# Performance work log

Hardware: AMD Instinct MI355X
Metric: run time of the kernel (lower is better)

Reference implementation:

```python
import jax, jax.numpy as jnp
import numpy as np
import itertools

GRID_SIZES = [0.01, 0.02, 0.04, 0.08, 0.16, 0.32, 0.64, 1.28]
OFFSETS = np.array(list(itertools.product([-1, 0, 1], repeat=3)), dtype=np.int32)  # [27,3]; index 13 = (0,0,0)
B, N, IN_DIM, HID, OUT_DIM = 2, 65536, 3, 32, 128


def make_neighbors(p, g):
    """Submanifold-conv neighbor tables for one grid scale.
    Returns nbr [27, b*n] int32 (flat point id or -1) and mask [27, b*n] bool.
    """
    b, n, _ = p.shape
    D = int(np.ceil(1.0 / g)) + 1  # static upper bound on spatial shape (p in [0,1))
    gc = jnp.floor(p / g).astype(jnp.int32)
    gc = gc - jnp.min(gc, axis=1, keepdims=True)  # per-batch min, as in torch code
    ids = jnp.arange(b * n, dtype=jnp.int32).reshape(b, n)
    bidx = jnp.arange(b, dtype=jnp.int32)[:, None]
    # deterministic voxel hash: one representative point id per occupied voxel
    grid = jnp.full((b, D, D, D), -1, jnp.int32)
    grid = grid.at[bidx, gc[..., 0], gc[..., 1], gc[..., 2]].max(ids)
    off = jnp.asarray(OFFSETS)
    nc = gc[None] + off[:, None, None, :]  # [27,b,n,3]
    valid = jnp.all((nc >= 0) & (nc < D), axis=-1)
    ncc = jnp.clip(nc, 0, D - 1)
    nbr = grid[bidx[None], ncc[..., 0], ncc[..., 1], ncc[..., 2]]  # [27,b,n]
    mask = valid & (nbr >= 0)
    nbr = nbr.at[13].set(ids)  # center tap is always the point itself
    mask = mask.at[13].set(True)
    return nbr.reshape(27, b * n), mask.reshape(27, b * n)


def subm_conv(f, W, bias, nbr, mask):
    """Submanifold 3x3x3 sparse conv on active sites.
    f [M,h]; W [27,h,h]; nbr/mask [27,M]. out[p] = bias + sum_k (f @ W_k)[nbr_k(p)] (masked).
    Scan over the 27 kernel taps keeps peak memory at O(M*h).
    """
    def step(acc, kin):
        Wk, nbrk, mk = kin
        acc = acc + jnp.where(mk[:, None], (f @ Wk)[nbrk], 0.0)
        return acc, None
    acc0 = jnp.zeros_like(f) + bias
    out, _ = jax.lax.scan(step, acc0, (W, nbr, mask))
    return out


def mssc_forward(p, w1, b1, w_mlp, b_mlp, w_conv, b_conv, w2, b2, neighbors):
    b, n, _ = p.shape
    pts = p @ w1 + b1  # mlp_1: [b,n,HID]
    outs = []
    for i in range(len(GRID_SIZES)):
        nbr, mask = neighbors[i]
        h0 = (pts @ w_mlp[i] + b_mlp[i]).reshape(b * n, HID)  # per-scale MLP
        h1 = subm_conv(h0, w_conv[2 * i], b_conv[2 * i], nbr, mask) + h0
        h2 = subm_conv(h1, w_conv[2 * i + 1], b_conv[2 * i + 1], nbr, mask) + h1
        outs.append(h2 + h0)  # features + features_batch residual
    feat = jnp.concatenate(outs, axis=1).reshape(b, n, HID * len(GRID_SIZES))
    return feat @ w2 + b2  # mlp_2


def setup_inputs():
    key = jax.random.key(0)
    ks = jax.random.split(key, 10)
    L = len(GRID_SIZES)
    return {
        "p": jax.random.uniform(ks[0], (B, N, IN_DIM), jnp.float32),
        "w1": jax.random.normal(ks[1], (IN_DIM, HID), jnp.float32) / np.sqrt(IN_DIM),
        "b1": 0.01 * jax.random.normal(ks[2], (HID,), jnp.float32),
        "w_mlp": jax.random.normal(ks[3], (L, HID, HID), jnp.float32) / np.sqrt(HID),
        "b_mlp": 0.01 * jax.random.normal(ks[4], (L, HID), jnp.float32),
        "w_conv": jax.random.normal(ks[5], (2 * L, 27, HID, HID), jnp.float32) / np.sqrt(27 * HID),
        "b_conv": 0.01 * jax.random.normal(ks[6], (2 * L, HID), jnp.float32),
        "w2": jax.random.normal(ks[7], (HID * L, OUT_DIM), jnp.float32) / np.sqrt(HID * L),
        "b2": 0.01 * jax.random.normal(ks[8], (OUT_DIM,), jnp.float32),
    }


def reference(p, w1, b1, w_mlp, b_mlp, w_conv, b_conv, w2, b2):
    neighbors = [make_neighbors(p, g) for g in GRID_SIZES]
    return mssc_forward(p, w1, b1, w_mlp, b_mlp, w_conv, b_conv, w2, b2, neighbors)
```

## Files before the change

### kernel.cpp

```cpp
#include <hip/hip_runtime.h>

#define MTOT 131072
#define NB   65536

typedef __attribute__((ext_vector_type(8))) __bf16 bf16x8;
typedef __attribute__((ext_vector_type(4))) __bf16 bf16x4;
typedef __attribute__((ext_vector_type(4))) float  f32x4;

__global__ void pmin_init_kernel(float* pmin){
    if (threadIdx.x < 6) pmin[threadIdx.x] = 2.0f;
}

__global__ void pmin_kernel(const float* __restrict__ p, float* __restrict__ pmin){
    int bi = blockIdx.y;
    float m0 = 2.f, m1 = 2.f, m2 = 2.f;
    for (int ni = blockIdx.x * blockDim.x + threadIdx.x; ni < NB; ni += gridDim.x * blockDim.x){
        const float* pp = p + ((size_t)bi * NB + ni) * 3;
        m0 = fminf(m0, pp[0]); m1 = fminf(m1, pp[1]); m2 = fminf(m2, pp[2]);
    }
    #pragma unroll
    for (int o = 32; o > 0; o >>= 1){
        m0 = fminf(m0, __shfl_down(m0, o, 64));
        m1 = fminf(m1, __shfl_down(m1, o, 64));
        m2 = fminf(m2, __shfl_down(m2, o, 64));
    }
    if ((threadIdx.x & 63) == 0){
        atomicMin((int*)(pmin + bi*3 + 0), __float_as_int(m0));
        atomicMin((int*)(pmin + bi*3 + 1), __float_as_int(m1));
        atomicMin((int*)(pmin + bi*3 + 2), __float_as_int(m2));
    }
}

template<int USE_LDS>
__global__ void scatter_kernel(const float* __restrict__ p, const float* __restrict__ pmin,
                               int* __restrict__ vgrid, int* __restrict__ gcbuf,
                               double gd, int D){
    extern __shared__ int lgrid[];
    int m  = blockIdx.x * blockDim.x + threadIdx.x;
    int bi = m >> 16;
    double px = (double)p[m*3], py = (double)p[m*3+1], pz = (double)p[m*3+2];
    int gx = (int)floor(px / gd) - (int)floor((double)pmin[bi*3+0] / gd);
    int gy = (int)floor(py / gd) - (int)floor((double)pmin[bi*3+1] / gd);
    int gz = (int)floor(pz / gd) - (int)floor((double)pmin[bi*3+2] / gd);
    gcbuf[m] = (gx << 20) | (gy << 10) | gz;
    int cell = (gx * D + gy) * D + gz;

    if (!USE_LDS){
        atomicMax(vgrid + bi * D * D * D + cell, m);
        return;
    }
    int ncell = D * D * D;
    for (int c = threadIdx.x; c < ncell; c += 256) lgrid[c] = -1;
    __syncthreads();
    atomicMax(&lgrid[cell], m);
    __syncthreads();
    int* vg = vgrid + bi * ncell;
    for (int c = threadIdx.x; c < ncell; c += 256){
        int v = lgrid[c];
        if (v >= 0) atomicMax(vg + c, v);
    }
}

__global__ void nbr_kernel(const int* __restrict__ gcbuf, const int* __restrict__ vgrid,
                           int* __restrict__ nbr, int D){
    int m  = blockIdx.x * blockDim.x + threadIdx.x;
    int bi = m >> 16;
    int pk = gcbuf[m];
    int gx = pk >> 20, gy = (pk >> 10) & 1023, gz = pk & 1023;
    #pragma unroll
    for (int k = 0; k < 27; k++){
        int v;
        if (k == 13){
            v = m;
        } else {
            int x = gx + (k/9) - 1;
            int y = gy + ((k/3)%3) - 1;
            int z = gz + (k%3) - 1;
            if (x < 0 || y < 0 || z < 0 || x >= D || y >= D || z >= D) v = -1;
            else v = vgrid[((bi * D + x) * D + y) * D + z];
        }
        nbr[k * MTOT + m] = v;
    }
}

__global__ void nbrv_kernel(const int* __restrict__ vgrid, int* __restrict__ nbrv,
                            int D, int NC2, int NC2pad){
    int ci = blockIdx.x * 256 + threadIdx.x;
    if (ci >= NC2pad) return;
    int D3 = D * D * D;
    int bi = (ci >= D3) ? 1 : 0;
    int r  = ci - bi * D3;
    int x = r / (D*D), y = (r / D) % D, z = r % D;
    #pragma unroll
    for (int k = 0; k < 27; k++){
        int v = -1;
        if (ci < NC2){
            int nx = x + (k/9) - 1;
            int ny = y + ((k/3)%3) - 1;
            int nz = z + (k%3) - 1;
            if (nx >= 0 && ny >= 0 && nz >= 0 && nx < D && ny < D && nz < D)
                v = vgrid[bi * D3 + ((nx * D + ny) * D + nz)];
        }
        nbrv[k * NC2pad + ci] = v;
    }
}

__global__ void wcv_wave_kernel(const float* __restrict__ w_conv,
                                __bf16* __restrict__ wth, __bf16* __restrict__ wtl){
    int o = blockIdx.x * 256 + threadIdx.x;
    int cv = o / 27648, r = o % 27648;
    int k = r / 1024, q = r % 1024;
    int half = q >> 9, t = q & 511;
    int l = t >> 3, e = t & 7;
    int c = half*16 + (l & 15);
    int j = (l >> 4)*8 + e;
    float x = w_conv[cv*27648 + k*1024 + j*32 + c];
    __bf16 hi = (__bf16)x;
    wth[o] = hi;
    wtl[o] = (__bf16)(x - (float)hi);
}

__global__ void wcv_kernel(const float* __restrict__ w_conv,
                           __bf16* __restrict__ wth, __bf16* __restrict__ wtl){
    int o = blockIdx.x * 256 + threadIdx.x;
    int cv = o / 27648, r = o % 27648;
    int k = r / 1024, q = r % 1024, c = q / 32, j = q % 32;
    float x = w_conv[cv*27648 + k*1024 + j*32 + c];
    __bf16 hi = (__bf16)x;
    wth[o] = hi;
    wtl[o] = (__bf16)(x - (float)hi);
}

__global__ void w2t_kernel(const float* __restrict__ w2,
                           __bf16* __restrict__ w2th, __bf16* __restrict__ w2tl){
    int o = blockIdx.x * 256 + threadIdx.x;
    int kc = o >> 12, r = o & 4095, c = r >> 5, j = r & 31;
    float x = w2[(kc*32 + j)*128 + c];
    __bf16 hi = (__bf16)x;
    w2th[o] = hi;
    w2tl[o] = (__bf16)(x - (float)hi);
}

__global__ void mlp_scale_kernel(const float* __restrict__ p, const float* __restrict__ w1,
                                 const float* __restrict__ b1,
                                 const float* __restrict__ w, const float* __restrict__ b,
                                 __bf16* __restrict__ h0h, __bf16* __restrict__ h0l){
    int t = blockIdx.x * blockDim.x + threadIdx.x;
    int c = t & 31, m = t >> 5;
    float x = p[m*3+0], y = p[m*3+1], z = p[m*3+2];
    float acc = b[c];
    #pragma unroll
    for (int j = 0; j < 32; j++){
        float ptsj = b1[j] + x * w1[j] + y * w1[32 + j] + z * w1[64 + j];
        acc += ptsj * w[j*32 + c];
    }
    __bf16 hi = (__bf16)acc;
    h0h[t] = hi;
    h0l[t] = (__bf16)(acc - (float)hi);
}

template<int MODE>
__global__ __launch_bounds__(256)
void conv4_kernel(const __bf16* __restrict__ fh, const __bf16* __restrict__ fl,
                  const __bf16* __restrict__ wth, const __bf16* __restrict__ wtl,
                  const float* __restrict__ bias, const int* __restrict__ nbr,
                  const __bf16* __restrict__ r2h, const __bf16* __restrict__ r2l,
                  __bf16* __restrict__ outh, __bf16* __restrict__ outl)
{
    __shared__ float buf0[32][33], buf1[32][33];
    int tid  = threadIdx.x;
    int lane = tid & 63, w = tid >> 6;
    int col  = lane & 15, kq = lane >> 4;
    int ptA  = blockIdx.x * 32 + col, ptB = ptA + 16;
    const int fragoff = kq * 8;

    f32x4 acc00, acc01, acc10, acc11;
    if (w == 0){
        float bv0 = bias[col], bv1 = bias[col + 16];
        acc00 = (f32x4){bv0,bv0,bv0,bv0}; acc01 = (f32x4){bv1,bv1,bv1,bv1};
        acc10 = (f32x4){bv0,bv0,bv0,bv0}; acc11 = (f32x4){bv1,bv1,bv1,bv1};
    } else {
        acc00 = (f32x4){0,0,0,0}; acc01 = (f32x4){0,0,0,0};
        acc10 = (f32x4){0,0,0,0}; acc11 = (f32x4){0,0,0,0};
    }

    int k0 = w * 7, k1 = (k0 + 7 < 27) ? k0 + 7 : 27;

    int idc = nbr[k0 * MTOT + ptA];
    int jdc = nbr[k0 * MTOT + ptB];
    int idn = (k0 + 1 < k1) ? nbr[(k0+1) * MTOT + ptA] : 0;
    int jdn = (k0 + 1 < k1) ? nbr[(k0+1) * MTOT + ptB] : 0;
    size_t oc0 = (size_t)(idc < 0 ? 0 : idc) * 32 + fragoff;
    size_t oc1 = (size_t)(jdc < 0 ? 0 : jdc) * 32 + fragoff;
    bf16x8 a0h = *(const bf16x8*)(fh + oc0);
    bf16x8 a0l = *(const bf16x8*)(fl + oc0);
    bf16x8 a1h = *(const bf16x8*)(fh + oc1);
    bf16x8 a1l = *(const bf16x8*)(fl + oc1);
    bool mc0 = idc < 0, mc1 = jdc < 0;

    #pragma unroll 1
    for (int k = k0; k < k1; k++){
        int idn2 = 0, jdn2 = 0;
        if (k + 2 < k1){ idn2 = nbr[(k+2) * MTOT + ptA]; jdn2 = nbr[(k+2) * MTOT + ptB]; }
        size_t on0 = (size_t)(idn < 0 ? 0 : idn) * 32 + fragoff;
        size_t on1 = (size_t)(jdn < 0 ? 0 : jdn) * 32 + fragoff;
        bf16x8 na0h = *(const bf16x8*)(fh + on0);
        bf16x8 na0l = *(const bf16x8*)(fl + on0);
        bf16x8 na1h = *(const bf16x8*)(fh + on1);
        bf16x8 na1l = *(const bf16x8*)(fl + on1);
        bool nm0 = idn < 0, nm1 = jdn < 0;

        const __bf16* wb = wth + (size_t)k*1024 + lane*8;
        const __bf16* wc = wtl + (size_t)k*1024 + lane*8;
        bf16x8 b0h = *(const bf16x8*)(wb);
        bf16x8 b1h = *(const bf16x8*)(wb + 512);
        bf16x8 b0l = *(const bf16x8*)(wc);
        bf16x8 b1l = *(const bf16x8*)(wc + 512);

        bf16x8 z = {};
        bf16x8 xa0h = mc0 ? z : a0h, xa0l = mc0 ? z : a0l;
        bf16x8 xa1h = mc1 ? z : a1h, xa1l = mc1 ? z : a1l;

        acc00 = __builtin_amdgcn_mfma_f32_16x16x32_bf16(xa0h, b0h, acc00, 0,0,0);
        acc00 = __builtin_amdgcn_mfma_f32_16x16x32_bf16(xa0h, b0l, acc00, 0,0,0);
        acc00 = __builtin_amdgcn_mfma_f32_16x16x32_bf16(xa0l, b0h, acc00, 0,0,0);
        acc01 = __builtin_amdgcn_mfma_f32_16x16x32_bf16(xa0h, b1h, acc01, 0,0,0);
        acc01 = __builtin_amdgcn_mfma_f32_16x16x32_bf16(xa0h, b1l, acc01, 0,0,0);
        acc01 = __builtin_amdgcn_mfma_f32_16x16x32_bf16(xa0l, b1h, acc01, 0,0,0);
        acc10 = __builtin_amdgcn_mfma_f32_16x16x32_bf16(xa1h, b0h, acc10, 0,0,0);
        acc10 = __builtin_amdgcn_mfma_f32_16x16x32_bf16(xa1h, b0l, acc10, 0,0,0);
        acc10 = __builtin_amdgcn_mfma_f32_16x16x32_bf16(xa1l, b0h, acc10, 0,0,0);
        acc11 = __builtin_amdgcn_mfma_f32_16x16x32_bf16(xa1h, b1h, acc11, 0,0,0);
        acc11 = __builtin_amdgcn_mfma_f32_16x16x32_bf16(xa1h, b1l, acc11, 0,0,0);
        acc11 = __builtin_amdgcn_mfma_f32_16x16x32_bf16(xa1l, b1h, acc11, 0,0,0);

        a0h = na0h; a0l = na0l; a1h = na1h; a1l = na1l;
        mc0 = nm0; mc1 = nm1; idn = idn2; jdn = jdn2;
    }

    if (w == 2){
        #pragma unroll
        for (int r = 0; r < 4; r++){
            buf0[kq*4 + r][col]           = acc00[r];
            buf0[kq*4 + r][col + 16]      = acc01[r];
            buf0[16 + kq*4 + r][col]      = acc10[r];
            buf0[16 + kq*4 + r][col + 16] = acc11[r];
        }
    } else if (w == 3){
        #pragma unroll
        for (int r = 0; r < 4; r++){
            buf1[kq*4 + r][col]           = acc00[r];
            buf1[kq*4 + r][col + 16]      = acc01[r];
            buf1[16 + kq*4 + r][col]      = acc10[r];
            buf1[16 + kq*4 + r][col + 16] = acc11[r];
        }
    }
    __syncthreads();
    if (w == 0){
        #pragma unroll
        for (int r = 0; r < 4; r++){
            acc00[r] += buf0[kq*4 + r][col];
            acc01[r] += buf0[kq*4 + r][col + 16];
            acc10[r] += buf0[16 + kq*4 + r][col];
            acc11[r] += buf0[16 + kq*4 + r][col + 16];
        }
    } else if (w == 1){
        #pragma unroll
        for (int r = 0; r < 4; r++){
            acc00[r] += buf1[kq*4 + r][col];
            acc01[r] += buf1[kq*4 + r][col + 16];
            acc10[r] += buf1[16 + kq*4 + r][col];
            acc11[r] += buf1[16 + kq*4 + r][col + 16];
        }
    }
    __syncthreads();
    if (w == 1){
        #pragma unroll
        for (int r = 0; r < 4; r++){
            buf1[kq*4 + r][col]           = acc00[r];
            buf1[kq*4 + r][col + 16]      = acc01[r];
            buf1[16 + kq*4 + r][col]      = acc10[r];
            buf1[16 + kq*4 + r][col + 16] = acc11[r];
        }
    }
    __syncthreads();
    if (w == 0){
        #pragma unroll
        for (int r = 0; r < 4; r++){
            buf0[kq*4 + r][col]           = acc00[r] + buf1[kq*4 + r][col];
            buf0[kq*4 + r][col + 16]      = acc01[r] + buf1[kq*4 + r][col + 16];
            buf0[16 + kq*4 + r][col]      = acc10[r] + buf1[16 + kq*4 + r][col];
            buf0[16 + kq*4 + r][col + 16] = acc11[r] + buf1[16 + kq*4 + r][col + 16];
        }
    }
    __syncthreads();

    int pt = tid >> 3, c0 = (tid & 7) * 4;
    size_t g = (size_t)(blockIdx.x * 32 + pt) * 32 + c0;
    bf16x4 rh = *(const bf16x4*)(fh + g);
    bf16x4 rl = *(const bf16x4*)(fl + g);
    bf16x4 oh4, ol4;
    if (MODE == 0){
        #pragma unroll
        for (int j = 0; j < 4; j++){
            float v = buf0[pt][c0 + j] + (float)rh[j] + (float)rl[j];
            __bf16 hi = (__bf16)v;
            oh4[j] = hi;
            ol4[j] = (__bf16)(v - (float)hi);
        }
    } else {
        bf16x4 sh = *(const bf16x4*)(r2h + g);
        bf16x4 sl = *(const bf16x4*)(r2l + g);
        #pragma unroll
        for (int j = 0; j < 4; j++){
            float v = buf0[pt][c0 + j] + (float)rh[j] + (float)rl[j]
                                       + (float)sh[j] + (float)sl[j];
            __bf16 hi = (__bf16)v;
            oh4[j] = hi;
            ol4[j] = (__bf16)(v - (float)hi);
        }
    }
    *(bf16x4*)(outh + g) = oh4;
    *(bf16x4*)(outl + g) = ol4;
}

__global__ __launch_bounds__(256)
void vconv_kernel(const __bf16* __restrict__ fh, const __bf16* __restrict__ fl,
                  const __bf16* __restrict__ wth, const __bf16* __restrict__ wtl,
                  const float* __restrict__ bias, const int* __restrict__ nbrv,
                  int NC2pad, float* __restrict__ vv)
{
    __shared__ float buf0[32][33], buf1[32][33];
    int tid  = threadIdx.x;
    int lane = tid & 63, w = tid >> 6;
    int col  = lane & 15, kq = lane >> 4;
    int ptA  = blockIdx.x * 32 + col, ptB = ptA + 16;
    const int fragoff = kq * 8;

    f32x4 acc00, acc01, acc10, acc11;
    if (w == 0){
        float bv0 = bias[col], bv1 = bias[col + 16];
        acc00 = (f32x4){bv0,bv0,bv0,bv0}; acc01 = (f32x4){bv1,bv1,bv1,bv1};
        acc10 = (f32x4){bv0,bv0,bv0,bv0}; acc11 = (f32x4){bv1,bv1,bv1,bv1};
    } else {
        acc00 = (f32x4){0,0,0,0}; acc01 = (f32x4){0,0,0,0};
        acc10 = (f32x4){0,0,0,0}; acc11 = (f32x4){0,0,0,0};
    }

    int k0 = (w == 0) ? 0 : (w == 1) ? 7 : (w == 2) ? 14 : 21;
    int k1 = (w == 0) ? 7 : (w == 1) ? 13 : (w == 2) ? 21 : 27;

    int idc = nbrv[k0 * NC2pad + ptA];
    int jdc = nbrv[k0 * NC2pad + ptB];
    int idn = (k0 + 1 < k1) ? nbrv[(k0+1) * NC2pad + ptA] : 0;
    int jdn = (k0 + 1 < k1) ? nbrv[(k0+1) * NC2pad + ptB] : 0;
    size_t oc0 = (size_t)(idc < 0 ? 0 : idc) * 32 + fragoff;
    size_t oc1 = (size_t)(jdc < 0 ? 0 : jdc) * 32 + fragoff;
    bf16x8 a0h = *(const bf16x8*)(fh + oc0);
    bf16x8 a0l = *(const bf16x8*)(fl + oc0);
    bf16x8 a1h = *(const bf16x8*)(fh + oc1);
    bf16x8 a1l = *(const bf16x8*)(fl + oc1);
    bool mc0 = idc < 0, mc1 = jdc < 0;

    #pragma unroll 1
    for (int k = k0; k < k1; k++){
        int idn2 = 0, jdn2 = 0;
        if (k + 2 < k1){ idn2 = nbrv[(k+2) * NC2pad + ptA]; jdn2 = nbrv[(k+2) * NC2pad + ptB]; }
        size_t on0 = (size_t)(idn < 0 ? 0 : idn) * 32 + fragoff;
        size_t on1 = (size_t)(jdn < 0 ? 0 : jdn) * 32 + fragoff;
        bf16x8 na0h = *(const bf16x8*)(fh + on0);
        bf16x8 na0l = *(const bf16x8*)(fl + on0);
        bf16x8 na1h = *(const bf16x8*)(fh + on1);
        bf16x8 na1l = *(const bf16x8*)(fl + on1);
        bool nm0 = idn < 0, nm1 = jdn < 0;

        const __bf16* wb = wth + (size_t)k*1024 + lane*8;
        const __bf16* wc = wtl + (size_t)k*1024 + lane*8;
        bf16x8 b0h = *(const bf16x8*)(wb);
        bf16x8 b1h = *(const bf16x8*)(wb + 512);
        bf16x8 b0l = *(const bf16x8*)(wc);
        bf16x8 b1l = *(const bf16x8*)(wc + 512);

        bf16x8 z = {};
        bf16x8 xa0h = mc0 ? z : a0h, xa0l = mc0 ? z : a0l;
        bf16x8 xa1h = mc1 ? z : a1h, xa1l = mc1 ? z : a1l;

        acc00 = __builtin_amdgcn_mfma_f32_16x16x32_bf16(xa0h, b0h, acc00, 0,0,0);
        acc00 = __builtin_amdgcn_mfma_f32_16x16x32_bf16(xa0h, b0l, acc00, 0,0,0);
        acc00 = __builtin_amdgcn_mfma_f32_16x16x32_bf16(xa0l, b0h, acc00, 0,0,0);
        acc01 = __builtin_amdgcn_mfma_f32_16x16x32_bf16(xa0h, b1h, acc01, 0,0,0);
        acc01 = __builtin_amdgcn_mfma_f32_16x16x32_bf16(xa0h, b1l, acc01, 0,0,0);
        acc01 = __builtin_amdgcn_mfma_f32_16x16x32_bf16(xa0l, b1h, acc01, 0,0,0);
        acc10 = __builtin_amdgcn_mfma_f32_16x16x32_bf16(xa1h, b0h, acc10, 0,0,0);
        acc10 = __builtin_amdgcn_mfma_f32_16x16x32_bf16(xa1h, b0l, acc10, 0,0,0);
        acc10 = __builtin_amdgcn_mfma_f32_16x16x32_bf16(xa1l, b0h, acc10, 0,0,0);
        acc11 = __builtin_amdgcn_mfma_f32_16x16x32_bf16(xa1h, b1h, acc11, 0,0,0);
        acc11 = __builtin_amdgcn_mfma_f32_16x16x32_bf16(xa1h, b1l, acc11, 0,0,0);
        acc11 = __builtin_amdgcn_mfma_f32_16x16x32_bf16(xa1l, b1h, acc11, 0,0,0);

        a0h = na0h; a0l = na0l; a1h = na1h; a1l = na1l;
        mc0 = nm0; mc1 = nm1; idn = idn2; jdn = jdn2;
    }

    if (w == 2){
        #pragma unroll
        for (int r = 0; r < 4; r++){
            buf0[kq*4 + r][col]           = acc00[r];
            buf0[kq*4 + r][col + 16]      = acc01[r];
            buf0[16 + kq*4 + r][col]      = acc10[r];
            buf0[16 + kq*4 + r][col + 16] = acc11[r];
        }
    } else if (w == 3){
        #pragma unroll
        for (int r = 0; r < 4; r++){
            buf1[kq*4 + r][col]           = acc00[r];
            buf1[kq*4 + r][col + 16]      = acc01[r];
            buf1[16 + kq*4 + r][col]      = acc10[r];
            buf1[16 + kq*4 + r][col + 16] = acc11[r];
        }
    }
    __syncthreads();
    if (w == 0){
        #pragma unroll
        for (int r = 0; r < 4; r++){
            acc00[r] += buf0[kq*4 + r][col];
            acc01[r] += buf0[kq*4 + r][col + 16];
            acc10[r] += buf0[16 + kq*4 + r][col];
            acc11[r] += buf0[16 + kq*4 + r][col + 16];
        }
    } else if (w == 1){
        #pragma unroll
        for (int r = 0; r < 4; r++){
            acc00[r] += buf1[kq*4 + r][col];
            acc01[r] += buf1[kq*4 + r][col + 16];
            acc10[r] += buf1[16 + kq*4 + r][col];
            acc11[r] += buf1[16 + kq*4 + r][col + 16];
        }
    }
    __syncthreads();
    if (w == 1){
        #pragma unroll
        for (int r = 0; r < 4; r++){
            buf1[kq*4 + r][col]           = acc00[r];
            buf1[kq*4 + r][col + 16]      = acc01[r];
            buf1[16 + kq*4 + r][col]      = acc10[r];
            buf1[16 + kq*4 + r][col + 16] = acc11[r];
        }
    }
    __syncthreads();
    if (w == 0){
        #pragma unroll
        for (int r = 0; r < 4; r++){
            buf0[kq*4 + r][col]           = acc00[r] + buf1[kq*4 + r][col];
            buf0[kq*4 + r][col + 16]      = acc01[r] + buf1[kq*4 + r][col + 16];
            buf0[16 + kq*4 + r][col]      = acc10[r] + buf1[16 + kq*4 + r][col];
            buf0[16 + kq*4 + r][col + 16] = acc11[r] + buf1[16 + kq*4 + r][col + 16];
        }
    }
    __syncthreads();

    int pt = tid >> 3, c0 = (tid & 7) * 4;
    float* o = vv + (size_t)(blockIdx.x * 32 + pt) * 32 + c0;
    ((float4*)o)[0] = make_float4(buf0[pt][c0], buf0[pt][c0+1], buf0[pt][c0+2], buf0[pt][c0+3]);
}

template<int MODE>
__global__ __launch_bounds__(256)
void combine_kernel(const __bf16* __restrict__ fh, const __bf16* __restrict__ fl,
                    const __bf16* __restrict__ wth, const __bf16* __restrict__ wtl,
                    const float* __restrict__ vv, const int* __restrict__ gcbuf, int D,
                    const __bf16* __restrict__ r2h, const __bf16* __restrict__ r2l,
                    __bf16* __restrict__ outh, __bf16* __restrict__ outl)
{
    __shared__ float vsh[128][33];
    int tid  = threadIdx.x;
    int lane = tid & 63, w = tid >> 6;
    int col  = lane & 15, kq = lane >> 4;
    const int fragoff = kq * 8;
    int mB  = blockIdx.x * 128 + w * 32;
    int ptA = mB + col, ptB = ptA + 16;

    size_t oA = (size_t)ptA * 32 + fragoff;
    size_t oB = (size_t)ptB * 32 + fragoff;
    bf16x8 a0h = *(const bf16x8*)(fh + oA);
    bf16x8 a0l = *(const bf16x8*)(fl + oA);
    bf16x8 a1h = *(const bf16x8*)(fh + oB);
    bf16x8 a1l = *(const bf16x8*)(fl + oB);

    const __bf16* wb = wth + 13*1024 + lane*8;
    const __bf16* wc = wtl + 13*1024 + lane*8;
    bf16x8 b0h = *(const bf16x8*)(wb);
    bf16x8 b1h = *(const bf16x8*)(wb + 512);
    bf16x8 b0l = *(const bf16x8*)(wc);
    bf16x8 b1l = *(const bf16x8*)(wc + 512);

    f32x4 acc00 = {0,0,0,0}, acc01 = {0,0,0,0}, acc10 = {0,0,0,0}, acc11 = {0,0,0,0};
    acc00 = __builtin_amdgcn_mfma_f32_16x16x32_bf16(a0h, b0h, acc00, 0,0,0);
    acc00 = __builtin_amdgcn_mfma_f32_16x16x32_bf16(a0h, b0l, acc00, 0,0,0);
    acc00 = __builtin_amdgcn_mfma_f32_16x16x32_bf16(a0l, b0h, acc00, 0,0,0);
    acc01 = __builtin_amdgcn_mfma_f32_16x16x32_bf16(a0h, b1h, acc01, 0,0,0);
    acc01 = __builtin_amdgcn_mfma_f32_16x16x32_bf16(a0h, b1l, acc01, 0,0,0);
    acc01 = __builtin_amdgcn_mfma_f32_16x16x32_bf16(a0l, b1h, acc01, 0,0,0);
    acc10 = __builtin_amdgcn_mfma_f32_16x16x32_bf16(a1h, b0h, acc10, 0,0,0);
    acc10 = __builtin_amdgcn_mfma_f32_16x16x32_bf16(a1h, b0l, acc10, 0,0,0);
    acc10 = __builtin_amdgcn_mfma_f32_16x16x32_bf16(a1l, b0h, acc10, 0,0,0);
    acc11 = __builtin_amdgcn_mfma_f32_16x16x32_bf16(a1h, b1h, acc11, 0,0,0);
    acc11 = __builtin_amdgcn_mfma_f32_16x16x32_bf16(a1h, b1l, acc11, 0,0,0);
    acc11 = __builtin_amdgcn_mfma_f32_16x16x32_bf16(a1l, b1h, acc11, 0,0,0);

    #pragma unroll
    for (int r = 0; r < 4; r++){
        vsh[w*32 + kq*4 + r][col]           = acc00[r];
        vsh[w*32 + kq*4 + r][col + 16]      = acc01[r];
        vsh[w*32 + 16 + kq*4 + r][col]      = acc10[r];
        vsh[w*32 + 16 + kq*4 + r][col + 16] = acc11[r];
    }
    __syncthreads();

    int pt = tid >> 1, c0 = (tid & 1) * 16;
    int m  = blockIdx.x * 128 + pt;
    int pk = gcbuf[m];
    int bi = m >> 16;
    int gx = pk >> 20, gy = (pk >> 10) & 1023, gz = pk & 1023;
    int ci = ((bi * D + gx) * D + gy) * D + gz;

    const float* vrow = vv + (size_t)ci * 32 + c0;
    size_t g = (size_t)m * 32 + c0;
    bf16x8 rh0 = *(const bf16x8*)(fh + g);
    bf16x8 rh1 = *(const bf16x8*)(fh + g + 8);
    bf16x8 rl0 = *(const bf16x8*)(fl + g);
    bf16x8 rl1 = *(const bf16x8*)(fl + g + 8);
    bf16x8 sh0, sh1, sl0, sl1;
    if (MODE == 1){
        sh0 = *(const bf16x8*)(r2h + g);
        sh1 = *(const bf16x8*)(r2h + g + 8);
        sl0 = *(const bf16x8*)(r2l + g);
        sl1 = *(const bf16x8*)(r2l + g + 8);
    }
    bf16x8 oh0, oh1, ol0, ol1;
    #pragma unroll
    for (int j = 0; j < 8; j++){
        float v = vsh[pt][c0 + j] + vrow[j] + (float)rh0[j] + (float)rl0[j];
        if (MODE == 1) v += (float)sh0[j] + (float)sl0[j];
        __bf16 hi = (__bf16)v;
        oh0[j] = hi; ol0[j] = (__bf16)(v - (float)hi);
    }
    #pragma unroll
    for (int j = 0; j < 8; j++){
        float v = vsh[pt][c0 + 8 + j] + vrow[8 + j] + (float)rh1[j] + (float)rl1[j];
        if (MODE == 1) v += (float)sh1[j] + (float)sl1[j];
        __bf16 hi = (__bf16)v;
        oh1[j] = hi; ol1[j] = (__bf16)(v - (float)hi);
    }
    *(bf16x8*)(outh + g)     = oh0;
    *(bf16x8*)(outh + g + 8) = oh1;
    *(bf16x8*)(outl + g)     = ol0;
    *(bf16x8*)(outl + g + 8) = ol1;
}

__global__ __launch_bounds__(256)
void mlp2_kernel(const __bf16* __restrict__ vplanes,
                 const __bf16* __restrict__ w2th, const __bf16* __restrict__ w2tl,
                 const float* __restrict__ b2, float* __restrict__ out)
{
    int tid  = threadIdx.x;
    int lane = tid & 63, w = tid >> 6;
    int col  = lane & 15, kq = lane >> 4;
    const int fragoff = kq * 8;
    int pbase = blockIdx.x * 128 + w * 32;
    size_t oA = (size_t)(pbase + col) * 32 + fragoff;
    size_t oB = (size_t)(pbase + 16 + col) * 32 + fragoff;

    f32x4 acc[4][4];
    #pragma unroll
    for (int s = 0; s < 4; s++)
        #pragma unroll
        for (int q = 0; q < 4; q++) acc[s][q] = (f32x4){0,0,0,0};

    bf16x8 a0h = *(const bf16x8*)(vplanes + oA);
    bf16x8 a0l = *(const bf16x8*)(vplanes + 4194304 + oA);
    bf16x8 a1h = *(const bf16x8*)(vplanes + oB);
    bf16x8 a1l = *(const bf16x8*)(vplanes + 4194304 + oB);

    #pragma unroll 1
    for (int kc = 0; kc < 8; kc++){
        bf16x8 na0h, na0l, na1h, na1l;
        if (kc < 7){
            const __bf16* fnh = vplanes + (size_t)(kc+1) * 8388608;
            const __bf16* fnl = fnh + 4194304;
            na0h = *(const bf16x8*)(fnh + oA);
            na0l = *(const bf16x8*)(fnl + oA);
            na1h = *(const bf16x8*)(fnh + oB);
            na1l = *(const bf16x8*)(fnl + oB);
        } else {
            na0h = a0h; na0l = a0l; na1h = a1h; na1l = a1l;
        }

        const __bf16* wbase  = w2th + (size_t)kc * 4096;
        const __bf16* wlbase = w2tl + (size_t)kc * 4096;
        #pragma unroll
        for (int s = 0; s < 4; s++){
            const __bf16* wb = wbase  + (s*32 + col) * 32 + fragoff;
            const __bf16* wc = wlbase + (s*32 + col) * 32 + fragoff;
            bf16x8 b0h = *(const bf16x8*)(wb);
            bf16x8 b1h = *(const bf16x8*)(wb + 512);
            bf16x8 b0l = *(const bf16x8*)(wc);
            bf16x8 b1l = *(const bf16x8*)(wc + 512);

            acc[s][0] = __builtin_amdgcn_mfma_f32_16x16x32_bf16(a0h, b0h, acc[s][0], 0,0,0);
            acc[s][0] = __builtin_amdgcn_mfma_f32_16x16x32_bf16(a0h, b0l, acc[s][0], 0,0,0);
            acc[s][0] = __builtin_amdgcn_mfma_f32_16x16x32_bf16(a0l, b0h, acc[s][0], 0,0,0);
            acc[s][1] = __builtin_amdgcn_mfma_f32_16x16x32_bf16(a0h, b1h, acc[s][1], 0,0,0);
            acc[s][1] = __builtin_amdgcn_mfma_f32_16x16x32_bf16(a0h, b1l, acc[s][1], 0,0,0);
            acc[s][1] = __builtin_amdgcn_mfma_f32_16x16x32_bf16(a0l, b1h, acc[s][1], 0,0,0);
            acc[s][2] = __builtin_amdgcn_mfma_f32_16x16x32_bf16(a1h, b0h, acc[s][2], 0,0,0);
            acc[s][2] = __builtin_amdgcn_mfma_f32_16x16x32_bf16(a1h, b0l, acc[s][2], 0,0,0);
            acc[s][2] = __builtin_amdgcn_mfma_f32_16x16x32_bf16(a1l, b0h, acc[s][2], 0,0,0);
            acc[s][3] = __builtin_amdgcn_mfma_f32_16x16x32_bf16(a1h, b1h, acc[s][3], 0,0,0);
            acc[s][3] = __builtin_amdgcn_mfma_f32_16x16x32_bf16(a1h, b1l, acc[s][3], 0,0,0);
            acc[s][3] = __builtin_amdgcn_mfma_f32_16x16x32_bf16(a1l, b1h, acc[s][3], 0,0,0);
        }

        a0h = na0h; a0l = na0l; a1h = na1h; a1l = na1l;
    }

    #pragma unroll
    for (int s = 0; s < 4; s++){
        float bl = b2[s*32 + col], bh = b2[s*32 + 16 + col];
        #pragma unroll
        for (int r = 0; r < 4; r++){
            size_t rowA = (size_t)(pbase + kq*4 + r) * 128;
            size_t rowB = (size_t)(pbase + 16 + kq*4 + r) * 128;
            out[rowA + s*32 + col]      = acc[s][0][r] + bl;
            out[rowA + s*32 + 16 + col] = acc[s][1][r] + bh;
            out[rowB + s*32 + col]      = acc[s][2][r] + bl;
            out[rowB + s*32 + 16 + col] = acc[s][3][r] + bh;
        }
    }
}

template<int MODE>
__global__ __launch_bounds__(256)
void conv_mfma_kernel(const __bf16* __restrict__ fh, const __bf16* __restrict__ fl,
                      const __bf16* __restrict__ wth, const __bf16* __restrict__ wtl,
                      const float* __restrict__ bias, const int* __restrict__ nbr,
                      const __bf16* __restrict__ r2h, const __bf16* __restrict__ r2l,
                      const float* __restrict__ w2i, const float* __restrict__ b2,
                      __bf16* __restrict__ outh, __bf16* __restrict__ outl,
                      float* __restrict__ out)
{
    __shared__ float vsh[64][33];
    int tid  = threadIdx.x;
    int lane = tid & 63, wid = tid >> 6;
    int pair = wid >> 1;
    int half = wid & 1;
    int col  = lane & 15, kq = lane >> 4;
    int m0   = blockIdx.x * 64 + pair * 32;
    int ptA  = m0 + col, ptB = ptA + 16;
    const int fragoff = kq * 8;

    f32x4 acc00, acc01, acc10, acc11;
    if (half == 0){
        float bv0 = bias[col], bv1 = bias[col + 16];
        acc00 = (f32x4){bv0,bv0,bv0,bv0}; acc01 = (f32x4){bv1,bv1,bv1,bv1};
        acc10 = (f32x4){bv0,bv0,bv0,bv0}; acc11 = (f32x4){bv1,bv1,bv1,bv1};
    } else {
        acc00 = (f32x4){0,0,0,0}; acc01 = (f32x4){0,0,0,0};
        acc10 = (f32x4){0,0,0,0}; acc11 = (f32x4){0,0,0,0};
    }

    int k0 = half ? 14 : 0;
    int k1 = half ? 27 : 14;
    #pragma unroll 1
    for (int k = k0; k < k1; k++){
        int nb0 = nbr[k * MTOT + ptA];
        int nb1 = nbr[k * MTOT + ptB];
        size_t o0 = (size_t)(nb0 < 0 ? 0 : nb0) * 32 + fragoff;
        size_t o1 = (size_t)(nb1 < 0 ? 0 : nb1) * 32 + fragoff;
        bf16x8 a0h = *(const bf16x8*)(fh + o0);
        bf16x8 a0l = *(const bf16x8*)(fl + o0);
        bf16x8 a1h = *(const bf16x8*)(fh + o1);
        bf16x8 a1l = *(const bf16x8*)(fl + o1);
        bf16x8 z = {};
        if (nb0 < 0){ a0h = z; a0l = z; }
        if (nb1 < 0){ a1h = z; a1l = z; }

        const __bf16* wb = wth + (size_t)k*1024 + col*32 + fragoff;
        const __bf16* wc = wtl + (size_t)k*1024 + col*32 + fragoff;
        bf16x8 b0h = *(const bf16x8*)(wb);
        bf16x8 b1h = *(const bf16x8*)(wb + 512);
        bf16x8 b0l = *(const bf16x8*)(wc);
        bf16x8 b1l = *(const bf16x8*)(wc + 512);

        acc00 = __builtin_amdgcn_mfma_f32_16x16x32_bf16(a0h, b0h, acc00, 0,0,0);
        acc00 = __builtin_amdgcn_mfma_f32_16x16x32_bf16(a0h, b0l, acc00, 0,0,0);
        acc00 = __builtin_amdgcn_mfma_f32_16x16x32_bf16(a0l, b0h, acc00, 0,0,0);
        acc01 = __builtin_amdgcn_mfma_f32_16x16x32_bf16(a0h, b1h, acc01, 0,0,0);
        acc01 = __builtin_amdgcn_mfma_f32_16x16x32_bf16(a0h, b1l, acc01, 0,0,0);
        acc01 = __builtin_amdgcn_mfma_f32_16x16x32_bf16(a0l, b1h, acc01, 0,0,0);
        acc10 = __builtin_amdgcn_mfma_f32_16x16x32_bf16(a1h, b0h, acc10, 0,0,0);
        acc10 = __builtin_amdgcn_mfma_f32_16x16x32_bf16(a1h, b0l, acc10, 0,0,0);
        acc10 = __builtin_amdgcn_mfma_f32_16x16x32_bf16(a1l, b0h, acc10, 0,0,0);
        acc11 = __builtin_amdgcn_mfma_f32_16x16x32_bf16(a1h, b1h, acc11, 0,0,0);
        acc11 = __builtin_amdgcn_mfma_f32_16x16x32_bf16(a1h, b1l, acc11, 0,0,0);
        acc11 = __builtin_amdgcn_mfma_f32_16x16x32_bf16(a1l, b1h, acc11, 0,0,0);
    }

    if (half == 1){
        #pragma unroll
        for (int r = 0; r < 4; r++){
            vsh[pair*32 + kq*4 + r][col]           = acc00[r];
            vsh[pair*32 + kq*4 + r][col + 16]      = acc01[r];
            vsh[pair*32 + 16 + kq*4 + r][col]      = acc10[r];
            vsh[pair*32 + 16 + kq*4 + r][col + 16] = acc11[r];
        }
    }
    __syncthreads();
    if (half == 0){
        #pragma unroll
        for (int r = 0; r < 4; r++){
            vsh[pair*32 + kq*4 + r][col]           += acc00[r];
            vsh[pair*32 + kq*4 + r][col + 16]      += acc01[r];
            vsh[pair*32 + 16 + kq*4 + r][col]      += acc10[r];
            vsh[pair*32 + 16 + kq*4 + r][col + 16] += acc11[r];
        }
    }
    __syncthreads();

    if (MODE == 0){
        int eidx = tid * 8;
        int pt = eidx >> 5, c0 = eidx & 31;
        size_t g = (size_t)blockIdx.x * 2048 + eidx;
        bf16x8 rh = *(const bf16x8*)(fh + g);
        bf16x8 rl = *(const bf16x8*)(fl + g);
        bf16x8 oh8, ol8;
        #pragma unroll
        for (int j = 0; j < 8; j++){
            float v = vsh[pt][c0 + j] + (float)rh[j] + (float)rl[j];
            __bf16 hi = (__bf16)v;
            oh8[j] = hi;
            ol8[j] = (__bf16)(v - (float)hi);
        }
        *(bf16x8*)(outh + g) = oh8;
        *(bf16x8*)(outl + g) = ol8;
    } else {
        int eidx = tid * 8;
        int pt = eidx >> 5, c0 = eidx & 31;
        size_t g = (size_t)blockIdx.x * 2048 + eidx;
        bf16x8 rh = *(const bf16x8*)(fh + g);
        bf16x8 rl = *(const bf16x8*)(fl + g);
        bf16x8 sh = *(const bf16x8*)(r2h + g);
        bf16x8 sl = *(const bf16x8*)(r2l + g);
        #pragma unroll
        for (int j = 0; j < 8; j++)
            vsh[pt][c0 + j] += (float)rh[j] + (float)rl[j] + (float)sh[j] + (float)sl[j];
        __syncthreads();

        int pm = tid & 63;
        int tg = __builtin_amdgcn_readfirstlane(tid >> 6);
        size_t m = (size_t)blockIdx.x * 64 + pm;
        float o32[32];
        float* obase = out + m*128 + tg*32;
        if (MODE == 2){
            #pragma unroll
            for (int o = 0; o < 32; o++) o32[o] = b2[tg*32 + o];
        } else {
            #pragma unroll
            for (int q = 0; q < 8; q++){
                float4 t4 = ((const float4*)obase)[q];
                o32[q*4+0] = t4.x; o32[q*4+1] = t4.y; o32[q*4+2] = t4.z; o32[q*4+3] = t4.w;
            }
        }
        #pragma unroll
        for (int c = 0; c < 32; c++){
            float vc = vsh[pm][c];
            const float* w2r = w2i + c*128 + tg*32;
            #pragma unroll
            for (int o = 0; o < 32; o++) o32[o] += vc * w2r[o];
        }
        #pragma unroll
        for (int q = 0; q < 8; q++)
            ((float4*)obase)[q] = make_float4(o32[q*4+0], o32[q*4+1], o32[q*4+2], o32[q*4+3]);
    }
}

extern "C" void kernel_launch(void* const* d_in, const int* in_sizes, int n_in,
                              void* d_out, int out_size, void* d_ws, size_t ws_size,
                              hipStream_t stream)
{
    static const int want[9] = {393216, 96, 32, 8192, 256, 442368, 512, 32768, 128};
    const void* bound[9];
    for (int i = 0; i < 9; i++) bound[i] = d_in[i];
    if (n_in == 9){
        for (int i = 0; i < 9; i++)
            for (int j = 0; j < 9; j++)
                if (in_sizes[j] == want[i]) { bound[i] = d_in[j]; break; }
    }
    const float* p      = (const float*)bound[0];
    const float* w1     = (const float*)bound[1];
    const float* b1     = (const float*)bound[2];
    const float* w_mlp  = (const float*)bound[3];
    const float* b_mlp  = (const float*)bound[4];
    const float* w_conv = (const float*)bound[5];
    const float* b_conv = (const float*)bound[6];
    const float* w2     = (const float*)bound[7];
    const float* b2     = (const float*)bound[8];
    float* out = (float*)d_out;

    char* ws = (char*)d_ws;
    __bf16* h0h  = (__bf16*)(ws);
    __bf16* h0l  = (__bf16*)(ws + 8388608);
    __bf16* h1h  = (__bf16*)(ws + 16777216);
    int*    vgrid= (int*)   (ws + 16777216);
    __bf16* h1l  = (__bf16*)(ws + 25165824);
    int*    nbr  = (int*)   (ws + 33554432);
    int*    nbrv = (int*)   (ws + 33554432);
    float*  vv   = (float*) (ws + 33554432 + 6291456);
    __bf16* wth  = (__bf16*)(ws + 47710208);
    __bf16* wtl  = (__bf16*)(ws + 48594944);
    __bf16* w2th = (__bf16*)(ws + 49479680);
    __bf16* w2tl = (__bf16*)(ws + 49545216);
    float*  pmin = (float*) (ws + 49610752);
    int*    gcbuf= (int*)   (ws + 49612800);
    __bf16* vpl  = (__bf16*)(ws + 50331648);

    const bool big = (ws_size >= 184549376ULL);

    static const double GS[8] = {0.01, 0.02, 0.04, 0.08, 0.16, 0.32, 0.64, 1.28};
    static const int    DS[8] = {101, 51, 26, 14, 8, 5, 3, 2};

    pmin_init_kernel<<<1, 64, 0, stream>>>(pmin);
    pmin_kernel<<<dim3(64, 2), 256, 0, stream>>>(p, pmin);
    if (big){
        wcv_wave_kernel<<<1728, 256, 0, stream>>>(w_conv, wth, wtl);
        w2t_kernel<<<128, 256, 0, stream>>>(w2, w2th, w2tl);
    } else {
        wcv_kernel<<<1728, 256, 0, stream>>>(w_conv, wth, wtl);
    }

    for (int i = 0; i < 8; i++){
        int D = DS[i]; double gd = GS[i];
        int ncell = D * D * D;
        int NC2 = 2 * ncell;
        hipMemsetAsync(vgrid, 0xFF, (size_t)NC2*sizeof(int), stream);
        if (ncell <= 2744)
            scatter_kernel<1><<<MTOT/256, 256, ncell*sizeof(int), stream>>>(p, pmin, vgrid, gcbuf, gd, D);
        else
            scatter_kernel<0><<<MTOT/256, 256, 0, stream>>>(p, pmin, vgrid, gcbuf, gd, D);

        const bool voxel = big && (NC2 < MTOT);

        if (voxel){
            int NC2pad = (NC2 + 31) & ~31;
            nbrv_kernel<<<(NC2pad + 255)/256, 256, 0, stream>>>(vgrid, nbrv, D, NC2, NC2pad);
            mlp_scale_kernel<<<(MTOT*32)/256, 256, 0, stream>>>(
                p, w1, b1, w_mlp + i*1024, b_mlp + i*32, h0h, h0l);
            vconv_kernel<<<NC2pad/32, 256, 0, stream>>>(
                h0h, h0l, wth + (size_t)(2*i)*27648, wtl + (size_t)(2*i)*27648,
                b_conv + (2*i)*32, nbrv, NC2pad, vv);
            combine_kernel<0><<<MTOT/128, 256, 0, stream>>>(
                h0h, h0l, wth + (size_t)(2*i)*27648, wtl + (size_t)(2*i)*27648,
                vv, gcbuf, D, nullptr, nullptr, h1h, h1l);
            vconv_kernel<<<NC2pad/32, 256, 0, stream>>>(
                h1h, h1l, wth + (size_t)(2*i+1)*27648, wtl + (size_t)(2*i+1)*27648,
                b_conv + (2*i+1)*32, nbrv, NC2pad, vv);
            combine_kernel<1><<<MTOT/128, 256, 0, stream>>>(
                h1h, h1l, wth + (size_t)(2*i+1)*27648, wtl + (size_t)(2*i+1)*27648,
                vv, gcbuf, D, h0h, h0l,
                vpl + (size_t)i*8388608, vpl + (size_t)i*8388608 + 4194304);
        } else {
            nbr_kernel<<<MTOT/256, 256, 0, stream>>>(gcbuf, vgrid, nbr, D);
            mlp_scale_kernel<<<(MTOT*32)/256, 256, 0, stream>>>(
                p, w1, b1, w_mlp + i*1024, b_mlp + i*32, h0h, h0l);
            if (big){
                conv4_kernel<0><<<MTOT/32, 256, 0, stream>>>(
                    h0h, h0l, wth + (size_t)(2*i)*27648, wtl + (size_t)(2*i)*27648,
                    b_conv + (2*i)*32, nbr, nullptr, nullptr, h1h, h1l);
                conv4_kernel<1><<<MTOT/32, 256, 0, stream>>>(
                    h1h, h1l, wth + (size_t)(2*i+1)*27648, wtl + (size_t)(2*i+1)*27648,
                    b_conv + (2*i+1)*32, nbr, h0h, h0l,
                    vpl + (size_t)i*8388608, vpl + (size_t)i*8388608 + 4194304);
            } else {
                conv_mfma_kernel<0><<<MTOT/64, 256, 0, stream>>>(
                    h0h, h0l, wth + (size_t)(2*i)*27648, wtl + (size_t)(2*i)*27648,
                    b_conv + (2*i)*32, nbr, nullptr, nullptr, nullptr, nullptr,
                    h1h, h1l, nullptr);
                if (i == 0)
                    conv_mfma_kernel<2><<<MTOT/64, 256, 0, stream>>>(
                        h1h, h1l, wth + (size_t)(2*i+1)*27648, wtl + (size_t)(2*i+1)*27648,
                        b_conv + (2*i+1)*32, nbr, h0h, h0l, w2 + i*32*128, b2,
                        nullptr, nullptr, out);
                else
                    conv_mfma_kernel<1><<<MTOT/64, 256, 0, stream>>>(
                        h1h, h1l, wth + (size_t)(2*i+1)*27648, wtl + (size_t)(2*i+1)*27648,
                        b_conv + (2*i+1)*32, nbr, h0h, h0l, w2 + i*32*128, nullptr,
                        nullptr, nullptr, out);
            }
        }
    }
    if (big)
        mlp2_kernel<<<MTOT/128, 256, 0, stream>>>(vpl, w2th, w2tl, b2, out);
}
```

Baseline: 848.3 us.

## Spatially sort points by coarse voxel bin to localize neighbor gathers

Adds a counting sort of points into a 51^3 per-batch spatial bin grid (histogram, single-block scan, atomic scatter) and runs all per-point feature buffers in sorted order. Neighbor tables are remapped through sortpos, and the final output writes are scattered back through origid. The aim is to make the 27-tap neighbor gathers in the conv kernels hit nearby memory, improving cache locality. It costs three extra kernels, a serial 1024-thread scan over about 265K bins, and indirect reads and scattered writes in the output stage. The sorted path only runs when the workspace is large enough.

```diff
diff --git a/kernel.cpp b/kernel.cpp
--- a/kernel.cpp
+++ b/kernel.cpp
@@ -2,6 +2,7 @@
 
 #define MTOT 131072
 #define NB   65536
+#define SNBINS 265302
 
 typedef __attribute__((ext_vector_type(8))) __bf16 bf16x8;
 typedef __attribute__((ext_vector_type(4))) __bf16 bf16x4;
@@ -29,6 +30,52 @@
         atomicMin((int*)(pmin + bi*3 + 1), __float_as_int(m1));
         atomicMin((int*)(pmin + bi*3 + 2), __float_as_int(m2));
     }
+}
+
+__device__ __forceinline__ int sort_bin(const float* __restrict__ p, int m){
+    int bi = m >> 16;
+    int gx = (int)(p[m*3+0] * 51.0f); gx = gx > 50 ? 50 : gx;
+    int gy = (int)(p[m*3+1] * 51.0f); gy = gy > 50 ? 50 : gy;
+    int gz = (int)(p[m*3+2] * 51.0f); gz = gz > 50 ? 50 : gz;
+    return bi * 132651 + (gx * 51 + gy) * 51 + gz;
+}
+
+__global__ void shist_kernel(const float* __restrict__ p, int* __restrict__ hist){
+    int m = blockIdx.x * 256 + threadIdx.x;
+    atomicAdd(hist + sort_bin(p, m), 1);
+}
+
+__global__ void sscan_kernel(const int* __restrict__ hist, int* __restrict__ offs){
+    __shared__ int sh[1024];
+    const int CH = 260;
+    int tid = threadIdx.x;
+    int base = tid * CH;
+    int sum = 0;
+    for (int i = 0; i < CH; i++){
+        int idx = base + i;
+        if (idx < SNBINS) sum += hist[idx];
+    }
+    sh[tid] = sum;
+    __syncthreads();
+    for (int off = 1; off < 1024; off <<= 1){
+        int v = (tid >= off) ? sh[tid - off] : 0;
+        __syncthreads();
+        sh[tid] += v;
+        __syncthreads();
+    }
+    int run = (tid == 0) ? 0 : sh[tid - 1];
+    for (int i = 0; i < CH; i++){
+        int idx = base + i;
+        if (idx < SNBINS){ offs[idx] = run; run += hist[idx]; }
+    }
+}
+
+__global__ void sscatter_kernel(const float* __restrict__ p, int* __restrict__ offs,
+                                int* __restrict__ sortpos, int* __restrict__ origid){
+    int m = blockIdx.x * 256 + threadIdx.x;
+    int pos = atomicAdd(offs + sort_bin(p, m), 1);
+    sortpos[m] = pos;
+    origid[pos] = m;
 }
 
 template<int USE_LDS>
@@ -62,8 +109,10 @@
 }
 
 __global__ void nbr_kernel(const int* __restrict__ gcbuf, const int* __restrict__ vgrid,
+                           const int* __restrict__ origid, const int* __restrict__ sortpos,
                            int* __restrict__ nbr, int D){
-    int m  = blockIdx.x * blockDim.x + threadIdx.x;
+    int s  = blockIdx.x * blockDim.x + threadIdx.x;
+    int m  = origid ? origid[s] : s;
     int bi = m >> 16;
     int pk = gcbuf[m];
     int gx = pk >> 20, gy = (pk >> 10) & 1023, gz = pk & 1023;
@@ -71,20 +120,23 @@
     for (int k = 0; k < 27; k++){
         int v;
         if (k == 13){
-            v = m;
+            v = s;
         } else {
             int x = gx + (k/9) - 1;
             int y = gy + ((k/3)%3) - 1;
             int z = gz + (k%3) - 1;
             if (x < 0 || y < 0 || z < 0 || x >= D || y >= D || z >= D) v = -1;
-            else v = vgrid[((bi * D + x) * D + y) * D + z];
-        }
-        nbr[k * MTOT + m] = v;
-    }
-}
-
-__global__ void nbrv_kernel(const int* __restrict__ vgrid, int* __restrict__ nbrv,
-                            int D, int NC2, int NC2pad){
+            else {
+                v = vgrid[((bi * D + x) * D + y) * D + z];
+                if (v >= 0 && sortpos) v = sortpos[v];
+            }
+        }
+        nbr[k * MTOT + s] = v;
+    }
+}
+
+__global__ void nbrv_kernel(const int* __restrict__ vgrid, const int* __restrict__ sortpos,
+                            int* __restrict__ nbrv, int D, int NC2, int NC2pad){
     int ci = blockIdx.x * 256 + threadIdx.x;
     if (ci >= NC2pad) return;
     int D3 = D * D * D;
@@ -98,8 +150,10 @@
             int nx = x + (k/9) - 1;
             int ny = y + ((k/3)%3) - 1;
             int nz = z + (k%3) - 1;
-            if (nx >= 0 && ny >= 0 && nz >= 0 && nx < D && ny < D && nz < D)
+            if (nx >= 0 && ny >= 0 && nz >= 0 && nx < D && ny < D && nz < D){
                 v = vgrid[bi * D3 + ((nx * D + ny) * D + nz)];
+                if (v >= 0 && sortpos) v = sortpos[v];
+            }
         }
         nbrv[k * NC2pad + ci] = v;
     }
@@ -141,12 +195,13 @@
     w2tl[o] = (__bf16)(x - (float)hi);
 }
 
-__global__ void mlp_scale_kernel(const float* __restrict__ p, const float* __restrict__ w1,
-                                 const float* __restrict__ b1,
+__global__ void mlp_scale_kernel(const float* __restrict__ p, const int* __restrict__ origid,
+                                 const float* __restrict__ w1, const float* __restrict__ b1,
                                  const float* __restrict__ w, const float* __restrict__ b,
                                  __bf16* __restrict__ h0h, __bf16* __restrict__ h0l){
     int t = blockIdx.x * blockDim.x + threadIdx.x;
-    int c = t & 31, m = t >> 5;
+    int c = t & 31, s = t >> 5;
+    int m = origid ? origid[s] : s;
     float x = p[m*3+0], y = p[m*3+1], z = p[m*3+2];
     float acc = b[c];
     #pragma unroll
@@ -468,7 +523,8 @@
 __global__ __launch_bounds__(256)
 void combine_kernel(const __bf16* __restrict__ fh, const __bf16* __restrict__ fl,
                     const __bf16* __restrict__ wth, const __bf16* __restrict__ wtl,
-                    const float* __restrict__ vv, const int* __restrict__ gcbuf, int D,
+                    const float* __restrict__ vv, const int* __restrict__ gcbuf,
+                    const int* __restrict__ origid, int D,
                     const __bf16* __restrict__ r2h, const __bf16* __restrict__ r2l,
                     __bf16* __restrict__ outh, __bf16* __restrict__ outl)
 {
@@ -518,14 +574,15 @@
     __syncthreads();
 
     int pt = tid >> 1, c0 = (tid & 1) * 16;
-    int m  = blockIdx.x * 128 + pt;
+    int s  = blockIdx.x * 128 + pt;
+    int m  = origid ? origid[s] : s;
     int pk = gcbuf[m];
     int bi = m >> 16;
     int gx = pk >> 20, gy = (pk >> 10) & 1023, gz = pk & 1023;
     int ci = ((bi * D + gx) * D + gy) * D + gz;
 
     const float* vrow = vv + (size_t)ci * 32 + c0;
-    size_t g = (size_t)m * 32 + c0;
+    size_t g = (size_t)s * 32 + c0;
     bf16x8 rh0 = *(const bf16x8*)(fh + g);
     bf16x8 rh1 = *(const bf16x8*)(fh + g + 8);
     bf16x8 rl0 = *(const bf16x8*)(fl + g);
@@ -561,7 +618,8 @@
 __global__ __launch_bounds__(256)
 void mlp2_kernel(const __bf16* __restrict__ vplanes,
                  const __bf16* __restrict__ w2th, const __bf16* __restrict__ w2tl,
-                 const float* __restrict__ b2, float* __restrict__ out)
+                 const float* __restrict__ b2, const int* __restrict__ origid,
+                 float* __restrict__ out)
 {
     int tid  = threadIdx.x;
     int lane = tid & 63, w = tid >> 6;
@@ -629,8 +687,10 @@
         float bl = b2[s*32 + col], bh = b2[s*32 + 16 + col];
         #pragma unroll
         for (int r = 0; r < 4; r++){
-            size_t rowA = (size_t)(pbase + kq*4 + r) * 128;
-            size_t rowB = (size_t)(pbase + 16 + kq*4 + r) * 128;
+            int iA = pbase + kq*4 + r;
+            int iB = pbase + 16 + kq*4 + r;
+            size_t rowA = (size_t)(origid ? origid[iA] : iA) * 128;
+            size_t rowB = (size_t)(origid ? origid[iB] : iB) * 128;
             out[rowA + s*32 + col]      = acc[s][0][r] + bl;
             out[rowA + s*32 + 16 + col] = acc[s][1][r] + bh;
             out[rowB + s*32 + col]      = acc[s][2][r] + bl;
@@ -823,8 +883,15 @@
     float*  pmin = (float*) (ws + 49610752);
     int*    gcbuf= (int*)   (ws + 49612800);
     __bf16* vpl  = (__bf16*)(ws + 50331648);
+    int*    hist = (int*)   (ws + 184549376);
+    int*    offs = (int*)   (ws + 185614336);
+    int*    sortpos=(int*)  (ws + 186679296);
+    int*    origid =(int*)  (ws + 187203584);
 
     const bool big = (ws_size >= 184549376ULL);
+    const bool srt = (ws_size >= 187727872ULL);
+    const int* oid = srt ? origid  : nullptr;
+    const int* spp = srt ? sortpos : nullptr;
 
     static const double GS[8] = {0.01, 0.02, 0.04, 0.08, 0.16, 0.32, 0.64, 1.28};
     static const int    DS[8] = {101, 51, 26, 14, 8, 5, 3, 2};
@@ -836,6 +903,12 @@
         w2t_kernel<<<128, 256, 0, stream>>>(w2, w2th, w2tl);
     } else {
         wcv_kernel<<<1728, 256, 0, stream>>>(w_conv, wth, wtl);
+    }
+    if (srt){
+        hipMemsetAsync(hist, 0, SNBINS*sizeof(int), stream);
+        shist_kernel<<<MTOT/256, 256, 0, stream>>>(p, hist);
+        sscan_kernel<<<1, 1024, 0, stream>>>(hist, offs);
+        sscatter_kernel<<<MTOT/256, 256, 0, stream>>>(p, offs, sortpos, origid);
     }
 
     for (int i = 0; i < 8; i++){
@@ -852,26 +925,26 @@
 
         if (voxel){
             int NC2pad = (NC2 + 31) & ~31;
-            nbrv_kernel<<<(NC2pad + 255)/256, 256, 0, stream>>>(vgrid, nbrv, D, NC2, NC2pad);
+            nbrv_kernel<<<(NC2pad + 255)/256, 256, 0, stream>>>(vgrid, spp, nbrv, D, NC2, NC2pad);
             mlp_scale_kernel<<<(MTOT*32)/256, 256, 0, stream>>>(
-                p, w1, b1, w_mlp + i*1024, b_mlp + i*32, h0h, h0l);
+                p, oid, w1, b1, w_mlp + i*1024, b_mlp + i*32, h0h, h0l);
             vconv_kernel<<<NC2pad/32, 256, 0, stream>>>(
                 h0h, h0l, wth + (size_t)(2*i)*27648, wtl + (size_t)(2*i)*27648,
                 b_conv + (2*i)*32, nbrv, NC2pad, vv);
             combine_kernel<0><<<MTOT/128, 256, 0, stream>>>(
                 h0h, h0l, wth + (size_t)(2*i)*27648, wtl + (size_t)(2*i)*27648,
-                vv, gcbuf, D, nullptr, nullptr, h1h, h1l);
+                vv, gcbuf, oid, D, nullptr, nullptr, h1h, h1l);
             vconv_kernel<<<NC2pad/32, 256, 0, stream>>>(
                 h1h, h1l, wth + (size_t)(2*i+1)*27648, wtl + (size_t)(2*i+1)*27648,
                 b_conv + (2*i+1)*32, nbrv, NC2pad, vv);
             combine_kernel<1><<<MTOT/128, 256, 0, stream>>>(
                 h1h, h1l, wth + (size_t)(2*i+1)*27648, wtl + (size_t)(2*i+1)*27648,
-                vv, gcbuf, D, h0h, h0l,
+                vv, gcbuf, oid, D, h0h, h0l,
                 vpl + (size_t)i*8388608, vpl + (size_t)i*8388608 + 4194304);
         } else {
-            nbr_kernel<<<MTOT/256, 256, 0, stream>>>(gcbuf, vgrid, nbr, D);
+            nbr_kernel<<<MTOT/256, 256, 0, stream>>>(gcbuf, vgrid, oid, spp, nbr, D);
             mlp_scale_kernel<<<(MTOT*32)/256, 256, 0, stream>>>(
-                p, w1, b1, w_mlp + i*1024, b_mlp + i*32, h0h, h0l);
+                p, oid, w1, b1, w_mlp + i*1024, b_mlp + i*32, h0h, h0l);
             if (big){
                 conv4_kernel<0><<<MTOT/32, 256, 0, stream>>>(
                     h0h, h0l, wth + (size_t)(2*i)*27648, wtl + (size_t)(2*i)*27648,
@@ -899,5 +972,5 @@
         }
     }
     if (big)
-        mlp2_kernel<<<MTOT/128, 256, 0, stream>>>(vpl, w2th, w2tl, b2, out);
-}
+        mlp2_kernel<<<MTOT/128, 256, 0, stream>>>(vpl, w2th, w2tl, b2, oid, out);
+}
```

Result: slower. 1.351 ms (+59.3%).
